# Optimization experiments

Measured on AMD Instinct MI355X. Metric: run time of the kernel, lower is better.

The kernel has to match this reference:

```python
import jax, jax.numpy as jnp
import numpy as np

FC = 2048      # fc_feat_size
VEMB = 512     # video_embedding_size
WEMB = 512     # word_embedding_size
H = 512        # lstm_hidden_size
A = 256        # att_hidden_size
TV = 32        # video_time_step
TC = 20        # caption_time_step
BC = 16        # batch_size_caption
RP = 32        # rp_num (proposals per caption)
B = BC * RP    # batch_size
GLOVE = 300


def setup_inputs() -> dict:
    key = jax.random.key(0)
    ks = jax.random.split(key, 12)
    def u(k, shape):
        return jax.random.uniform(k, shape, jnp.float32, -0.1, 0.1)
    def n(k, shape, s=0.05):
        return jax.random.normal(k, shape, jnp.float32) * s
    return {
        "video_fc_feat": jax.random.normal(ks[0], (B, TV, FC), jnp.float32),
        "video_caption": jax.random.normal(ks[1], (BC, TC, GLOVE), jnp.float32),
        "cap_length_list": jax.random.randint(ks[2], (BC,), 0, TC),
        # video_embedding / word_embedding (Linear layers)
        "W_vemb": u(ks[3], (VEMB, FC)), "b_vemb": jnp.zeros((VEMB,), jnp.float32),
        "W_wemb": u(ks[4], (WEMB, GLOVE)), "b_wemb": jnp.zeros((WEMB,), jnp.float32),
        # LSTMCell for video (gate order i,f,g,o as in torch)
        "Wih_v": n(ks[5], (4 * H, VEMB)), "Whh_v": n(ks[6], (4 * H, H)),
        "bih_v": jnp.zeros((4 * H,), jnp.float32), "bhh_v": jnp.zeros((4 * H,), jnp.float32),
        # LSTMCell for caption
        "Wih_c": n(ks[7], (4 * H, WEMB)), "Whh_c": n(ks[8], (4 * H, H)),
        "bih_c": jnp.zeros((4 * H,), jnp.float32), "bhh_c": jnp.zeros((4 * H,), jnp.float32),
        # attention linears
        "W_vid": u(ks[9], (A, H)), "b_vid": jnp.zeros((A,), jnp.float32),
        "W_sen": u(ks[10], (A, H)), "b_sen": jnp.zeros((A,), jnp.float32),
        "W_att": u(ks[11], (1, A)), "b_att": jnp.zeros((1,), jnp.float32),
    }


def _lstm(x_seq, Wih, Whh, bih, bhh):
    # x_seq: [B, T, D] -> hidden states [B, T, H]; torch LSTMCell gate order i,f,g,o
    Bb = x_seq.shape[0]
    Hh = Whh.shape[1]
    def step(carry, x):
        h, c = carry
        g = x @ Wih.T + bih + h @ Whh.T + bhh
        i, f, gg, o = jnp.split(g, 4, axis=-1)
        c = jax.nn.sigmoid(f) * c + jax.nn.sigmoid(i) * jnp.tanh(gg)
        h = jax.nn.sigmoid(o) * jnp.tanh(c)
        return (h, c), h
    init = (jnp.zeros((Bb, Hh), x_seq.dtype), jnp.zeros((Bb, Hh), x_seq.dtype))
    _, hs = jax.lax.scan(step, init, jnp.swapaxes(x_seq, 0, 1))
    return jnp.swapaxes(hs, 0, 1)


def reference(video_fc_feat, video_caption, cap_length_list,
              W_vemb, b_vemb, W_wemb, b_wemb,
              Wih_v, Whh_v, bih_v, bhh_v,
              Wih_c, Whh_c, bih_c, bhh_c,
              W_vid, b_vid, W_sen, b_sen, W_att, b_att):
    Bb, TVv, _ = video_fc_feat.shape
    BCc, TCc, _ = video_caption.shape
    rp = Bb // BCc
    Hh = Whh_v.shape[1]

    # caption LSTM over embedded GloVe words
    cap_x = video_caption @ W_wemb.T + b_wemb                 # [BC, TC, WEMB]
    cap_h = _lstm(cap_x, Wih_c, Whh_c, bih_c, bhh_c)          # [BC, TC, H]
    # video LSTM over embedded fc features
    vid_x = video_fc_feat @ W_vemb.T + b_vemb                 # [B, TV, VEMB]
    vid_h = _lstm(vid_x, Wih_v, Whh_v, bih_v, bhh_v)          # [B, TV, H]

    # additive attention: tanh(vid_linear(h_v) + sen_linear(h_c)) -> att_linear
    c_lin = cap_h @ W_sen.T + b_sen                           # [BC, TC, A]
    v_lin = (vid_h @ W_vid.T + b_vid).reshape(BCc, rp, TVv, -1)  # [BC, RP, TV, A]
    scores = (jnp.tanh(v_lin[:, :, :, None, :] + c_lin[:, None, None, :, :])
              @ W_att.T + b_att)[..., 0]                      # [BC, RP, TV, TC]

    # ragged masked softmax over caption length (max(len, 1) as in original)
    cap_len = jnp.maximum(cap_length_list, 1)
    mask = jnp.arange(TCc)[None, :] < cap_len[:, None]        # [BC, TC]
    m = mask[:, None, None, :]
    w = jax.nn.softmax(jnp.where(m, scores, -1e9), axis=-1)
    w = jnp.where(m, w, 0.0)                                  # [BC, RP, TV, TC]

    att_cap = jnp.einsum('brvt,bth->brvh', w, cap_h)          # [BC, RP, TV, H]
    cap_ftr_mean = att_cap.mean(axis=2)                       # mean over video steps
    vid_mean = vid_h.mean(axis=1).reshape(BCc, rp, Hh)
    return (vid_mean, cap_ftr_mean)
```

## Files before the change

### kernel.cpp

```cpp
#include <hip/hip_runtime.h>
#include <hip/hip_bf16.h>

#define FCD 2048
#define VEMBD 512
#define WEMBD 512
#define HD 512
#define AD 256
#define TVD 32
#define TCD 20
#define BCD 16
#define RPD 32
#define BD 512
#define GLOVED 300

typedef __attribute__((ext_vector_type(8))) short short8v;
typedef __attribute__((ext_vector_type(4))) float f32x4;

__device__ __forceinline__ float sigf(float x) { return 1.0f / (1.0f + __expf(-x)); }
__device__ __forceinline__ float tanhfast(float x) {
    float e = __expf(2.0f * x);
    return 1.0f - 2.0f / (e + 1.0f);
}
__device__ __forceinline__ unsigned short f2bf(float x) {
    union { __hip_bfloat16 h; unsigned short u; } v;
    v.h = __float2bfloat16(x);
    return v.u;
}
__device__ __forceinline__ float b2f(unsigned short u) {
    union { unsigned int i; float f; } v;
    v.i = ((unsigned int)u) << 16;
    return v.f;
}

__launch_bounds__(256)
__global__ void conv_f2b_kernel(const float* __restrict__ src,
                                unsigned short* __restrict__ dst, int n4) {
    for (int i = blockIdx.x * 256 + threadIdx.x; i < n4; i += gridDim.x * 256) {
        const float4 v = ((const float4*)src)[i];
        ushort4 o;
        o.x = f2bf(v.x); o.y = f2bf(v.y); o.z = f2bf(v.z); o.w = f2bf(v.w);
        ((ushort4*)dst)[i] = o;
    }
}

__launch_bounds__(256)
__global__ void conv_wcat_perm_kernel(const float* __restrict__ Wih,
                                      const float* __restrict__ Whh,
                                      unsigned short* __restrict__ Wcat) {
    const int gp = blockIdx.x;
    const int q = (gp >> 4) & 3;
    const int hc = (gp >> 6) * 16 + (gp & 15);
    const long g = (long)(q * 512 + hc);
    for (int k = threadIdx.x; k < 512; k += 256) {
        Wcat[(long)gp * 1024 + k]       = f2bf(Wih[g * 512 + k]);
        Wcat[(long)gp * 1024 + 512 + k] = f2bf(Whh[g * 512 + k]);
    }
}

__launch_bounds__(256)
__global__ void conv_bsum_kernel(const float* __restrict__ bih,
                                 const float* __restrict__ bhh,
                                 float* __restrict__ bsum) {
    const int gp = blockIdx.x * 256 + threadIdx.x;
    if (gp < 2048) {
        const int q = (gp >> 4) & 3;
        const int hc = (gp >> 6) * 16 + (gp & 15);
        const int g = q * 512 + hc;
        bsum[gp] = bih[g] + bhh[g];
    }
}

template<int AF32, int OBF>
__launch_bounds__(256)
__global__ void mfma_gemm128(const void* __restrict__ A,
                             const unsigned short* __restrict__ Bw,
                             const float* __restrict__ bias,
                             void* __restrict__ Cout,
                             int M, int N, int K)
{
    __shared__ unsigned short As[128][72];
    __shared__ unsigned short Bs[128][72];
    const int m0 = blockIdx.x * 128;
    const int n0 = blockIdx.y * 128;
    const int tid = threadIdx.x;
    const int lane = tid & 63;
    const int wid = tid >> 6;
    const int wm = (wid >> 1) * 64;
    const int wn = (wid & 1) * 64;
    const int lrow = lane & 15;
    const int lko = (lane >> 4) * 8;
    const int sr = tid >> 1;
    const int sc = (tid & 1) * 32;

    f32x4 acc[4][4] = {};

    const float* Arow_f = (const float*)A + (long)(m0 + sr) * K;
    const unsigned short* Arow_b = (const unsigned short*)A + (long)(m0 + sr) * K;
    const unsigned short* Brow = Bw + (long)(n0 + sr) * K;

    if (AF32) {
#pragma unroll
        for (int i = 0; i < 8; i++) {
            const float4 v = *(const float4*)(Arow_f + sc + i * 4);
            unsigned short* d = &As[sr][sc + i * 4];
            d[0] = f2bf(v.x); d[1] = f2bf(v.y); d[2] = f2bf(v.z); d[3] = f2bf(v.w);
        }
    } else {
#pragma unroll
        for (int i = 0; i < 4; i++)
            *(short8v*)&As[sr][sc + i * 8] = *(const short8v*)(Arow_b + sc + i * 8);
    }
#pragma unroll
    for (int i = 0; i < 4; i++)
        *(short8v*)&Bs[sr][sc + i * 8] = *(const short8v*)(Brow + sc + i * 8);
    __syncthreads();

    const int nc = K >> 6;
    float4 paf[8];
    short8v pab[4], pb[4];
    for (int c = 0; c < nc; c++) {
        if (c < nc - 1) {
            const int k0 = (c + 1) * 64;
            if (AF32) {
#pragma unroll
                for (int i = 0; i < 8; i++)
                    paf[i] = *(const float4*)(Arow_f + k0 + sc + i * 4);
            } else {
#pragma unroll
                for (int i = 0; i < 4; i++)
                    pab[i] = *(const short8v*)(Arow_b + k0 + sc + i * 8);
            }
#pragma unroll
            for (int i = 0; i < 4; i++)
                pb[i] = *(const short8v*)(Brow + k0 + sc + i * 8);
        }
#pragma unroll
        for (int kk = 0; kk < 2; kk++) {
            short8v a[4], b[4];
#pragma unroll
            for (int mi = 0; mi < 4; mi++)
                a[mi] = *(const short8v*)&As[wm + mi * 16 + lrow][kk * 32 + lko];
#pragma unroll
            for (int ni = 0; ni < 4; ni++)
                b[ni] = *(const short8v*)&Bs[wn + ni * 16 + lrow][kk * 32 + lko];
#pragma unroll
            for (int mi = 0; mi < 4; mi++)
#pragma unroll
                for (int ni = 0; ni < 4; ni++)
                    acc[mi][ni] = __builtin_amdgcn_mfma_f32_16x16x32_bf16(
                        a[mi], b[ni], acc[mi][ni], 0, 0, 0);
        }
        __syncthreads();
        if (c < nc - 1) {
            if (AF32) {
#pragma unroll
                for (int i = 0; i < 8; i++) {
                    unsigned short* d = &As[sr][sc + i * 4];
                    d[0] = f2bf(paf[i].x); d[1] = f2bf(paf[i].y);
                    d[2] = f2bf(paf[i].z); d[3] = f2bf(paf[i].w);
                }
            } else {
#pragma unroll
                for (int i = 0; i < 4; i++)
                    *(short8v*)&As[sr][sc + i * 8] = pab[i];
            }
#pragma unroll
            for (int i = 0; i < 4; i++)
                *(short8v*)&Bs[sr][sc + i * 8] = pb[i];
            __syncthreads();
        }
    }

    const int rbase = (lane >> 4) * 4;
#pragma unroll
    for (int ni = 0; ni < 4; ni++) {
        const int col = n0 + wn + ni * 16 + lrow;
        const float bv = bias[col];
#pragma unroll
        for (int mi = 0; mi < 4; mi++) {
#pragma unroll
            for (int j = 0; j < 4; j++) {
                const long row = m0 + wm + mi * 16 + rbase + j;
                const float val = acc[mi][ni][j] + bv;
                if (OBF) ((unsigned short*)Cout)[row * N + col] = f2bf(val);
                else     ((float*)Cout)[row * N + col] = val;
            }
        }
    }
}

__launch_bounds__(512)
__global__ void step_fused(const unsigned short* __restrict__ vx,
                           const unsigned short* __restrict__ h_in,
                           unsigned short* __restrict__ h_out,
                           const unsigned short* __restrict__ Wcat,
                           const float* __restrict__ bsum,
                           float* __restrict__ c_state,
                           unsigned short* __restrict__ vid_h,
                           int t,
                           const float* __restrict__ xg,
                           const float* __restrict__ Whh_c,
                           const float* __restrict__ bhh_c,
                           const float* __restrict__ hc_in,
                           float* __restrict__ hc_out,
                           float* __restrict__ cap_cst,
                           float* __restrict__ cap_h)
{
    __shared__ __align__(16) unsigned char smem[69632];
    const int bx = blockIdx.x;
    const int tid = threadIdx.x;

    if (bx >= 256) {
        const int h0 = (bx - 256) * 16;
        float* Wsc = (float*)smem;
        float* Hshc = (float*)(smem + 17408);
        const int lrow = tid >> 3;
        const int lq8 = tid & 7;
        const int tx = tid & 15;
        const int ty = (tid >> 4) & 15;
        float acc4[4] = {};

        for (int k0 = 0; k0 < 512; k0 += 64) {
            {
                const int q = lrow >> 4;
                const int hcc = lrow & 15;
                const float* src = Whh_c + (long)(q * 512 + h0 + hcc) * 512 + k0 + lq8 * 8;
                const int col = hcc * 4 + q;
#pragma unroll
                for (int j = 0; j < 2; j++) {
                    const float4 v = *(const float4*)(src + j * 4);
                    Wsc[(lq8 * 8 + j * 4 + 0) * 68 + col] = v.x;
                    Wsc[(lq8 * 8 + j * 4 + 1) * 68 + col] = v.y;
                    Wsc[(lq8 * 8 + j * 4 + 2) * 68 + col] = v.z;
                    Wsc[(lq8 * 8 + j * 4 + 3) * 68 + col] = v.w;
                }
            }
            if (tid < 256) {
                const int lb = tid >> 4;
                const int lk4 = (tid & 15) * 4;
                *(float4*)&Hshc[lb * 68 + lk4] = *(const float4*)(hc_in + (long)lb * 512 + k0 + lk4);
            }
            __syncthreads();
            if (tid < 256) {
#pragma unroll
                for (int kq = 0; kq < 16; kq++) {
                    const float4 h4 = *(const float4*)&Hshc[ty * 68 + kq * 4];
                    const float4 w0 = *(const float4*)&Wsc[(kq * 4 + 0) * 68 + tx * 4];
                    const float4 w1 = *(const float4*)&Wsc[(kq * 4 + 1) * 68 + tx * 4];
                    const float4 w2 = *(const float4*)&Wsc[(kq * 4 + 2) * 68 + tx * 4];
                    const float4 w3 = *(const float4*)&Wsc[(kq * 4 + 3) * 68 + tx * 4];
                    acc4[0] += h4.x * w0.x + h4.y * w1.x + h4.z * w2.x + h4.w * w3.x;
                    acc4[1] += h4.x * w0.y + h4.y * w1.y + h4.z * w2.y + h4.w * w3.y;
                    acc4[2] += h4.x * w0.z + h4.y * w1.z + h4.z * w2.z + h4.w * w3.z;
                    acc4[3] += h4.x * w0.w + h4.y * w1.w + h4.z * w2.w + h4.w * w3.w;
                }
            }
            __syncthreads();
        }
        if (tid < 256) {
            const int hc = h0 + tx;
            const long xrow = (long)(ty * TCD + t) * 2048;
            const float gi = acc4[0] + xg[xrow + hc]        + bhh_c[hc];
            const float gf = acc4[1] + xg[xrow + 512 + hc]  + bhh_c[512 + hc];
            const float gg = acc4[2] + xg[xrow + 1024 + hc] + bhh_c[1024 + hc];
            const float go = acc4[3] + xg[xrow + 1536 + hc] + bhh_c[1536 + hc];
            const float c_old = cap_cst[(long)ty * 512 + hc];
            const float ii = sigf(gi), ff = sigf(gf), g2 = tanhfast(gg), oo = sigf(go);
            const float c = ff * c_old + ii * g2;
            const float h = oo * tanhfast(c);
            cap_cst[(long)ty * 512 + hc] = c;
            hc_out[(long)ty * 512 + hc] = h;
            cap_h[(long)(ty * TCD + t) * 512 + hc] = h;
        }
        return;
    }

    const int n0 = (bx & 31) * 64;
    const int b0 = (bx >> 5) * 64;
    const int lane = tid & 63;
    const int wl = (tid >> 6) & 3;
    const int g = tid >> 8;
    const int lrow = lane & 15;
    const int lko = (lane >> 4) * 8;
    const int sr = tid >> 3;
    const int sc = (tid & 7) * 16;

    unsigned short* As0 = (unsigned short*)smem;
    unsigned short* Ws0 = (unsigned short*)(smem + 17408);
    unsigned short* As1 = (unsigned short*)(smem + 34816);
    unsigned short* Ws1 = (unsigned short*)(smem + 52224);
    unsigned short* Asg = (unsigned short*)(smem + g * 34816);
    unsigned short* Wsg = Asg + 17408 / 2;

    const unsigned short* arow_vx = vx + ((long)(b0 + sr) * TVD + t) * 512;
    const unsigned short* arow_h  = h_in + (long)(b0 + sr) * 512;
    const unsigned short* wrow    = Wcat + (long)(n0 + sr) * 1024;

    f32x4 acc[4] = {};

#pragma unroll
    for (int i = 0; i < 2; i++) {
        *(short8v*)&As0[sr * 136 + sc + i * 8] = *(const short8v*)(arow_vx + sc + i * 8);
        *(short8v*)&Ws0[sr * 136 + sc + i * 8] = *(const short8v*)(wrow + sc + i * 8);
        *(short8v*)&As1[sr * 136 + sc + i * 8] = *(const short8v*)(arow_h + sc + i * 8);
        *(short8v*)&Ws1[sr * 136 + sc + i * 8] = *(const short8v*)(wrow + 512 + sc + i * 8);
    }
    __syncthreads();

    short8v pa0[2], pw0[2], pa1[2], pw1[2];
    for (int p = 0; p < 4; p++) {
        if (p < 3) {
            const int k0 = (p + 1) * 128;
#pragma unroll
            for (int i = 0; i < 2; i++) {
                pa0[i] = *(const short8v*)(arow_vx + k0 + sc + i * 8);
                pw0[i] = *(const short8v*)(wrow + k0 + sc + i * 8);
                pa1[i] = *(const short8v*)(arow_h + k0 + sc + i * 8);
                pw1[i] = *(const short8v*)(wrow + 512 + k0 + sc + i * 8);
            }
        }
#pragma unroll
        for (int kk = 0; kk < 4; kk++) {
            const short8v a = *(const short8v*)&Asg[(wl * 16 + lrow) * 136 + kk * 32 + lko];
#pragma unroll
            for (int ni = 0; ni < 4; ni++) {
                const short8v b = *(const short8v*)&Wsg[(ni * 16 + lrow) * 136 + kk * 32 + lko];
                acc[ni] = __builtin_amdgcn_mfma_f32_16x16x32_bf16(a, b, acc[ni], 0, 0, 0);
            }
        }
        __syncthreads();
        if (p < 3) {
#pragma unroll
            for (int i = 0; i < 2; i++) {
                *(short8v*)&As0[sr * 136 + sc + i * 8] = pa0[i];
                *(short8v*)&Ws0[sr * 136 + sc + i * 8] = pw0[i];
                *(short8v*)&As1[sr * 136 + sc + i * 8] = pa1[i];
                *(short8v*)&Ws1[sr * 136 + sc + i * 8] = pw1[i];
            }
            __syncthreads();
        }
    }

    float* red = (float*)(smem + 34816);
    const int flat = wl * 64 + lane;
    if (g == 1) {
#pragma unroll
        for (int ni = 0; ni < 4; ni++)
#pragma unroll
            for (int j = 0; j < 4; j++)
                red[(ni * 4 + j) * 256 + flat] = acc[ni][j];
    }
    __syncthreads();
    if (g == 0) {
        const int hc = (n0 >> 2) + lrow;
        const int rbase = (lane >> 4) * 4;
        const float bs0 = bsum[n0 + lrow];
        const float bs1 = bsum[n0 + 16 + lrow];
        const float bs2 = bsum[n0 + 32 + lrow];
        const float bs3 = bsum[n0 + 48 + lrow];
#pragma unroll
        for (int j = 0; j < 4; j++) {
            const long b = b0 + wl * 16 + rbase + j;
            const float gi = acc[0][j] + red[(0 * 4 + j) * 256 + flat] + bs0;
            const float gf = acc[1][j] + red[(1 * 4 + j) * 256 + flat] + bs1;
            const float gg = acc[2][j] + red[(2 * 4 + j) * 256 + flat] + bs2;
            const float go = acc[3][j] + red[(3 * 4 + j) * 256 + flat] + bs3;
            const float c_old = c_state[b * 512 + hc];
            const float ii = sigf(gi), ff = sigf(gf), g2 = tanhfast(gg), oo = sigf(go);
            const float cn = ff * c_old + ii * g2;
            const float h = oo * tanhfast(cn);
            c_state[b * 512 + hc] = cn;
            h_out[b * 512 + hc] = f2bf(h);
            vid_h[(b * TVD + t) * 512 + hc] = f2bf(h);
        }
    }
}

__launch_bounds__(256)
__global__ void gemm_bias_kernel(const float* __restrict__ A,
                                 const float* __restrict__ Bw,
                                 const float* __restrict__ bias,
                                 float* __restrict__ C,
                                 int M, int N, int K) {
    __shared__ float As[16][68];
    __shared__ float Bs[16][68];
    const int n0 = blockIdx.x * 64;
    const int m0 = blockIdx.y * 64;
    const int tid = threadIdx.x;
    const int tx = tid & 15;
    const int ty = tid >> 4;
    const int lrow = tid >> 2;
    const int lk4 = (tid & 3) * 4;

    float acc[4][4] = {};

    for (int k0 = 0; k0 < K; k0 += 16) {
        {
            const float* src = A + (long)(m0 + lrow) * K + k0 + lk4;
            float4 v;
            if (k0 + 16 <= K) v = *(const float4*)src;
            else {
                v.x = (k0 + lk4 + 0 < K) ? src[0] : 0.f;
                v.y = (k0 + lk4 + 1 < K) ? src[1] : 0.f;
                v.z = (k0 + lk4 + 2 < K) ? src[2] : 0.f;
                v.w = (k0 + lk4 + 3 < K) ? src[3] : 0.f;
            }
            As[lk4 + 0][lrow] = v.x; As[lk4 + 1][lrow] = v.y;
            As[lk4 + 2][lrow] = v.z; As[lk4 + 3][lrow] = v.w;
        }
        {
            const float* src = Bw + (long)(n0 + lrow) * K + k0 + lk4;
            float4 v;
            if (k0 + 16 <= K) v = *(const float4*)src;
            else {
                v.x = (k0 + lk4 + 0 < K) ? src[0] : 0.f;
                v.y = (k0 + lk4 + 1 < K) ? src[1] : 0.f;
                v.z = (k0 + lk4 + 2 < K) ? src[2] : 0.f;
                v.w = (k0 + lk4 + 3 < K) ? src[3] : 0.f;
            }
            Bs[lk4 + 0][lrow] = v.x; Bs[lk4 + 1][lrow] = v.y;
            Bs[lk4 + 2][lrow] = v.z; Bs[lk4 + 3][lrow] = v.w;
        }
        __syncthreads();
#pragma unroll
        for (int kk = 0; kk < 16; kk++) {
            const float4 av = *(const float4*)&As[kk][ty * 4];
            const float4 bv = *(const float4*)&Bs[kk][tx * 4];
            acc[0][0] += av.x * bv.x; acc[0][1] += av.x * bv.y; acc[0][2] += av.x * bv.z; acc[0][3] += av.x * bv.w;
            acc[1][0] += av.y * bv.x; acc[1][1] += av.y * bv.y; acc[1][2] += av.y * bv.z; acc[1][3] += av.y * bv.w;
            acc[2][0] += av.z * bv.x; acc[2][1] += av.z * bv.y; acc[2][2] += av.z * bv.z; acc[2][3] += av.z * bv.w;
            acc[3][0] += av.w * bv.x; acc[3][1] += av.w * bv.y; acc[3][2] += av.w * bv.z; acc[3][3] += av.w * bv.w;
        }
        __syncthreads();
    }

    const float b0v = bias[n0 + tx * 4 + 0];
    const float b1v = bias[n0 + tx * 4 + 1];
    const float b2v = bias[n0 + tx * 4 + 2];
    const float b3v = bias[n0 + tx * 4 + 3];
#pragma unroll
    for (int i = 0; i < 4; i++) {
        float* dst = C + (long)(m0 + ty * 4 + i) * N + n0 + tx * 4;
        dst[0] = acc[i][0] + b0v;
        dst[1] = acc[i][1] + b1v;
        dst[2] = acc[i][2] + b2v;
        dst[3] = acc[i][3] + b3v;
    }
}

__launch_bounds__(256)
__global__ void attn_kernel(const float* __restrict__ v_lin,
                            const float* __restrict__ c_lin,
                            const float* __restrict__ W_att,
                            const float* __restrict__ b_att,
                            const int* __restrict__ cap_len,
                            float* __restrict__ wbar)
{
    const int br = blockIdx.x;
    const int bc = br >> 5;
    const int tid = threadIdx.x;
    const int lane = tid & 63;
    const int wv = tid >> 6;
    __shared__ float cl[TCD][AD];
    __shared__ float vl[AD];
    __shared__ float sl[TVD][TCD];

    for (int tt = 0; tt < TCD; tt++)
        cl[tt][tid] = c_lin[(long)(bc * TCD + tt) * AD + tid];
    const float wa0 = W_att[lane];
    const float wa1 = W_att[64 + lane];
    const float wa2 = W_att[128 + lane];
    const float wa3 = W_att[192 + lane];
    const float batt = b_att[0];
    __syncthreads();

    for (int v = 0; v < TVD; v++) {
        vl[tid] = v_lin[((long)br * TVD + v) * AD + tid];
        __syncthreads();
        const float v0 = vl[lane], v1 = vl[64 + lane], v2 = vl[128 + lane], v3 = vl[192 + lane];
#pragma unroll
        for (int dt = 0; dt < 5; dt++) {
            const int t = wv * 5 + dt;
            float s = tanhfast(v0 + cl[t][lane]) * wa0
                    + tanhfast(v1 + cl[t][64 + lane]) * wa1
                    + tanhfast(v2 + cl[t][128 + lane]) * wa2
                    + tanhfast(v3 + cl[t][192 + lane]) * wa3;
            for (int off = 32; off > 0; off >>= 1) s += __shfl_down(s, off, 64);
            if (lane == 0) sl[v][t] = s + batt;
        }
        __syncthreads();
    }

    int L = cap_len[bc];
    if (L < 1) L = 1;
    if (tid < TVD) {
        const int v = tid;
        float m = -1e30f;
        for (int t = 0; t < TCD; t++)
            if (t < L) m = fmaxf(m, sl[v][t]);
        float sum = 0.f;
        for (int t = 0; t < TCD; t++)
            if (t < L) sum += __expf(sl[v][t] - m);
        const float inv = 1.f / sum;
        for (int t = 0; t < TCD; t++)
            sl[v][t] = (t < L) ? __expf(sl[v][t] - m) * inv : 0.f;
    }
    __syncthreads();
    if (tid < TCD) {
        float s = 0.f;
        for (int v = 0; v < TVD; v++) s += sl[v][tid];
        wbar[(long)br * TCD + tid] = s * (1.0f / TVD);
    }
}

__launch_bounds__(256)
__global__ void capftr_kernel(const float* __restrict__ wbar,
                              const float* __restrict__ cap_h,
                              float* __restrict__ out2)
{
    const int idx = blockIdx.x * 256 + threadIdx.x;
    const int h = idx & 511;
    const int br = idx >> 9;
    const int bc = br >> 5;
    float s = 0.f;
#pragma unroll
    for (int t = 0; t < TCD; t++)
        s += wbar[br * TCD + t] * cap_h[(long)(bc * TCD + t) * HD + h];
    out2[idx] = s;
}

__launch_bounds__(256)
__global__ void vidmean_bf_kernel(const unsigned short* __restrict__ vid_h,
                                  float* __restrict__ out1)
{
    const int idx = blockIdx.x * 256 + threadIdx.x;
    const int b = idx >> 6;
    const int h8 = (idx & 63) * 8;
    float s[8] = {};
    for (int t = 0; t < TVD; t++) {
        const short8v v = *(const short8v*)(vid_h + ((long)b * TVD + t) * 512 + h8);
#pragma unroll
        for (int j = 0; j < 8; j++) s[j] += b2f((unsigned short)v[j]);
    }
#pragma unroll
    for (int j = 0; j < 8; j++)
        out1[(long)b * 512 + h8 + j] = s[j] * (1.0f / TVD);
}

extern "C" void kernel_launch(void* const* d_in, const int* in_sizes, int n_in,
                              void* d_out, int out_size, void* d_ws, size_t ws_size,
                              hipStream_t stream) {
    const float* video_fc      = (const float*)d_in[0];
    const float* video_caption = (const float*)d_in[1];
    const int*   cap_len       = (const int*)d_in[2];
    const float* W_vemb = (const float*)d_in[3];
    const float* b_vemb = (const float*)d_in[4];
    const float* W_wemb = (const float*)d_in[5];
    const float* b_wemb = (const float*)d_in[6];
    const float* Wih_v  = (const float*)d_in[7];
    const float* Whh_v  = (const float*)d_in[8];
    const float* bih_v  = (const float*)d_in[9];
    const float* bhh_v  = (const float*)d_in[10];
    const float* Wih_c  = (const float*)d_in[11];
    const float* Whh_c  = (const float*)d_in[12];
    const float* bih_c  = (const float*)d_in[13];
    const float* bhh_c  = (const float*)d_in[14];
    const float* W_vid  = (const float*)d_in[15];
    const float* b_vid  = (const float*)d_in[16];
    const float* W_sen  = (const float*)d_in[17];
    const float* b_sen  = (const float*)d_in[18];
    const float* W_att  = (const float*)d_in[19];
    const float* b_att  = (const float*)d_in[20];

    float* out1 = (float*)d_out;
    float* out2 = out1 + BD * HD;

    float* ws = (float*)d_ws;
    size_t off = 0;
    auto alloc = [&](size_t nfloats) {
        float* p = ws + off;
        off += (nfloats + 63) & ~(size_t)63;
        return p;
    };
    unsigned short* vidx_bf = (unsigned short*)alloc((size_t)BD * TVD * VEMBD / 2);
    unsigned short* vidh_bf = (unsigned short*)alloc((size_t)BD * TVD * HD / 2);
    unsigned short* h_bf_a  = (unsigned short*)alloc((size_t)BD * HD / 2);
    unsigned short* h_bf_b  = (unsigned short*)alloc((size_t)BD * HD / 2);
    float* c_st    = alloc((size_t)BD * HD);
    float* v_lin   = alloc((size_t)BD * TVD * AD);
    unsigned short* Wvemb_bf = (unsigned short*)alloc((size_t)VEMBD * FCD / 2);
    unsigned short* Wvid_bf  = (unsigned short*)alloc((size_t)AD * HD / 2);
    unsigned short* Wcat_bf  = (unsigned short*)alloc((size_t)2048 * 1024 / 2);
    float* bsum    = alloc(2048);
    float* cap_x   = alloc((size_t)BCD * TCD * WEMBD);
    float* xg_c    = alloc((size_t)BCD * TCD * 4 * HD);
    float* cap_h   = alloc((size_t)BCD * TCD * HD);
    float* c_lin   = alloc((size_t)BCD * TCD * AD);
    float* wbar    = alloc((size_t)BD * TCD);
    float* cap_ha  = alloc((size_t)BCD * HD);
    float* cap_hb  = alloc((size_t)BCD * HD);
    float* cap_cst = alloc((size_t)BCD * HD);

    hipMemsetAsync(h_bf_a, 0, (size_t)BD * HD * sizeof(unsigned short), stream);
    hipMemsetAsync(c_st, 0, (size_t)BD * HD * sizeof(float), stream);
    hipMemsetAsync(cap_ha, 0, (size_t)BCD * HD * sizeof(float), stream);
    hipMemsetAsync(cap_cst, 0, (size_t)BCD * HD * sizeof(float), stream);

    conv_f2b_kernel<<<512, 256, 0, stream>>>(W_vemb, Wvemb_bf, VEMBD * FCD / 4);
    conv_f2b_kernel<<<128, 256, 0, stream>>>(W_vid, Wvid_bf, AD * HD / 4);
    conv_wcat_perm_kernel<<<2048, 256, 0, stream>>>(Wih_v, Whh_v, Wcat_bf);
    conv_bsum_kernel<<<8, 256, 0, stream>>>(bih_v, bhh_v, bsum);

    gemm_bias_kernel<<<dim3(WEMBD / 64, (BCD * TCD) / 64), 256, 0, stream>>>(
        video_caption, W_wemb, b_wemb, cap_x, BCD * TCD, WEMBD, GLOVED);
    gemm_bias_kernel<<<dim3((4 * HD) / 64, (BCD * TCD) / 64), 256, 0, stream>>>(
        cap_x, Wih_c, bih_c, xg_c, BCD * TCD, 4 * HD, WEMBD);

    mfma_gemm128<1, 1><<<dim3((BD * TVD) / 128, VEMBD / 128), 256, 0, stream>>>(
        video_fc, Wvemb_bf, b_vemb, vidx_bf, BD * TVD, VEMBD, FCD);

    for (int t = 0; t < TVD; t++) {
        const unsigned short* hin = (t & 1) ? h_bf_b : h_bf_a;
        unsigned short* hout = (t & 1) ? h_bf_a : h_bf_b;
        const float* chin = (t & 1) ? cap_hb : cap_ha;
        float* chout = (t & 1) ? cap_ha : cap_hb;
        const int nblk = (t < TCD) ? 288 : 256;
        step_fused<<<nblk, 512, 0, stream>>>(
            vidx_bf, hin, hout, Wcat_bf, bsum, c_st, vidh_bf, t,
            xg_c, Whh_c, bhh_c, chin, chout, cap_cst, cap_h);
    }

    gemm_bias_kernel<<<dim3(AD / 64, (BCD * TCD) / 64), 256, 0, stream>>>(
        cap_h, W_sen, b_sen, c_lin, BCD * TCD, AD, HD);
    mfma_gemm128<0, 0><<<dim3((BD * TVD) / 128, AD / 128), 256, 0, stream>>>(
        vidh_bf, Wvid_bf, b_vid, v_lin, BD * TVD, AD, HD);

    attn_kernel<<<BD, 256, 0, stream>>>(v_lin, c_lin, W_att, b_att, cap_len, wbar);
    capftr_kernel<<<(BD * HD) / 256, 256, 0, stream>>>(wbar, cap_h, out2);
    vidmean_bf_kernel<<<(BD * HD / 8) / 256, 256, 0, stream>>>(vidh_bf, out1);
}
```

Before: 884.2 us.

## Shrink LSTM step blocks to 256 threads, fuse capftr into attention, preconvert fc feats

The recurrent step kernel moves from 512-thread blocks with a split-K reduction over 64-row tiles to 256-thread blocks on 32-row batch tiles. Each wave now owns distinct output columns, and the smem footprint drops so two blocks fit per CU. The caption-feature weighted sum is folded into the attention kernel, removing one launch and the wbar buffer. When workspace allows, video_fc is converted to bf16 first so the embedding GEMM reads bf16 input, at the cost of an extra conversion pass over a large tensor.

New measurement: 847.5 us. -4.1%, faster.

```diff
diff --git a/kernel.cpp b/kernel.cpp
--- a/kernel.cpp
+++ b/kernel.cpp
@@ -189,7 +189,7 @@
     }
 }
 
-__launch_bounds__(512)
+__launch_bounds__(256, 2)
 __global__ void step_fused(const unsigned short* __restrict__ vx,
                            const unsigned short* __restrict__ h_in,
                            unsigned short* __restrict__ h_out,
@@ -206,165 +206,157 @@
                            float* __restrict__ cap_cst,
                            float* __restrict__ cap_h)
 {
-    __shared__ __align__(16) unsigned char smem[69632];
+    __shared__ __align__(16) unsigned char smem[26112];
     const int bx = blockIdx.x;
     const int tid = threadIdx.x;
 
-    if (bx >= 256) {
-        const int h0 = (bx - 256) * 16;
+    if (bx >= 512) {
+        const int h0 = (bx - 512) * 16;
         float* Wsc = (float*)smem;
         float* Hshc = (float*)(smem + 17408);
-        const int lrow = tid >> 3;
-        const int lq8 = tid & 7;
         const int tx = tid & 15;
-        const int ty = (tid >> 4) & 15;
+        const int ty = tid >> 4;
+        const int lrow2 = tid >> 2;
+        const int lq = tid & 3;
         float acc4[4] = {};
 
         for (int k0 = 0; k0 < 512; k0 += 64) {
             {
-                const int q = lrow >> 4;
-                const int hcc = lrow & 15;
-                const float* src = Whh_c + (long)(q * 512 + h0 + hcc) * 512 + k0 + lq8 * 8;
+                const int q = lrow2 >> 4;
+                const int hcc = lrow2 & 15;
+                const float* src = Whh_c + (long)(q * 512 + h0 + hcc) * 512 + k0 + lq * 16;
                 const int col = hcc * 4 + q;
 #pragma unroll
-                for (int j = 0; j < 2; j++) {
+                for (int j = 0; j < 4; j++) {
                     const float4 v = *(const float4*)(src + j * 4);
-                    Wsc[(lq8 * 8 + j * 4 + 0) * 68 + col] = v.x;
-                    Wsc[(lq8 * 8 + j * 4 + 1) * 68 + col] = v.y;
-                    Wsc[(lq8 * 8 + j * 4 + 2) * 68 + col] = v.z;
-                    Wsc[(lq8 * 8 + j * 4 + 3) * 68 + col] = v.w;
+                    Wsc[(lq * 16 + j * 4 + 0) * 68 + col] = v.x;
+                    Wsc[(lq * 16 + j * 4 + 1) * 68 + col] = v.y;
+                    Wsc[(lq * 16 + j * 4 + 2) * 68 + col] = v.z;
+                    Wsc[(lq * 16 + j * 4 + 3) * 68 + col] = v.w;
                 }
             }
-            if (tid < 256) {
+            {
                 const int lb = tid >> 4;
                 const int lk4 = (tid & 15) * 4;
                 *(float4*)&Hshc[lb * 68 + lk4] = *(const float4*)(hc_in + (long)lb * 512 + k0 + lk4);
             }
             __syncthreads();
-            if (tid < 256) {
-#pragma unroll
-                for (int kq = 0; kq < 16; kq++) {
-                    const float4 h4 = *(const float4*)&Hshc[ty * 68 + kq * 4];
-                    const float4 w0 = *(const float4*)&Wsc[(kq * 4 + 0) * 68 + tx * 4];
-                    const float4 w1 = *(const float4*)&Wsc[(kq * 4 + 1) * 68 + tx * 4];
-                    const float4 w2 = *(const float4*)&Wsc[(kq * 4 + 2) * 68 + tx * 4];
-                    const float4 w3 = *(const float4*)&Wsc[(kq * 4 + 3) * 68 + tx * 4];
-                    acc4[0] += h4.x * w0.x + h4.y * w1.x + h4.z * w2.x + h4.w * w3.x;
-                    acc4[1] += h4.x * w0.y + h4.y * w1.y + h4.z * w2.y + h4.w * w3.y;
-                    acc4[2] += h4.x * w0.z + h4.y * w1.z + h4.z * w2.z + h4.w * w3.z;
-                    acc4[3] += h4.x * w0.w + h4.y * w1.w + h4.z * w2.w + h4.w * w3.w;
-                }
+#pragma unroll
+            for (int kq = 0; kq < 16; kq++) {
+                const float4 h4 = *(const float4*)&Hshc[ty * 68 + kq * 4];
+                const float4 w0 = *(const float4*)&Wsc[(kq * 4 + 0) * 68 + tx * 4];
+                const float4 w1 = *(const float4*)&Wsc[(kq * 4 + 1) * 68 + tx * 4];
+                const float4 w2 = *(const float4*)&Wsc[(kq * 4 + 2) * 68 + tx * 4];
+                const float4 w3 = *(const float4*)&Wsc[(kq * 4 + 3) * 68 + tx * 4];
+                acc4[0] += h4.x * w0.x + h4.y * w1.x + h4.z * w2.x + h4.w * w3.x;
+                acc4[1] += h4.x * w0.y + h4.y * w1.y + h4.z * w2.y + h4.w * w3.y;
+                acc4[2] += h4.x * w0.z + h4.y * w1.z + h4.z * w2.z + h4.w * w3.z;
+                acc4[3] += h4.x * w0.w + h4.y * w1.w + h4.z * w2.w + h4.w * w3.w;
             }
             __syncthreads();
         }
-        if (tid < 256) {
-            const int hc = h0 + tx;
-            const long xrow = (long)(ty * TCD + t) * 2048;
-            const float gi = acc4[0] + xg[xrow + hc]        + bhh_c[hc];
-            const float gf = acc4[1] + xg[xrow + 512 + hc]  + bhh_c[512 + hc];
-            const float gg = acc4[2] + xg[xrow + 1024 + hc] + bhh_c[1024 + hc];
-            const float go = acc4[3] + xg[xrow + 1536 + hc] + bhh_c[1536 + hc];
-            const float c_old = cap_cst[(long)ty * 512 + hc];
-            const float ii = sigf(gi), ff = sigf(gf), g2 = tanhfast(gg), oo = sigf(go);
-            const float c = ff * c_old + ii * g2;
-            const float h = oo * tanhfast(c);
-            cap_cst[(long)ty * 512 + hc] = c;
-            hc_out[(long)ty * 512 + hc] = h;
-            cap_h[(long)(ty * TCD + t) * 512 + hc] = h;
-        }
+        const int hc = h0 + tx;
+        const long xrow = (long)(ty * TCD + t) * 2048;
+        const float gi = acc4[0] + xg[xrow + hc]        + bhh_c[hc];
+        const float gf = acc4[1] + xg[xrow + 512 + hc]  + bhh_c[512 + hc];
+        const float gg = acc4[2] + xg[xrow + 1024 + hc] + bhh_c[1024 + hc];
+        const float go = acc4[3] + xg[xrow + 1536 + hc] + bhh_c[1536 + hc];
+        const float c_old = cap_cst[(long)ty * 512 + hc];
+        const float ii = sigf(gi), ff = sigf(gf), g2 = tanhfast(gg), oo = sigf(go);
+        const float c = ff * c_old + ii * g2;
+        const float h = oo * tanhfast(c);
+        cap_cst[(long)ty * 512 + hc] = c;
+        hc_out[(long)ty * 512 + hc] = h;
+        cap_h[(long)(ty * TCD + t) * 512 + hc] = h;
         return;
     }
 
     const int n0 = (bx & 31) * 64;
-    const int b0 = (bx >> 5) * 64;
+    const int b0 = (bx >> 5) * 32;
     const int lane = tid & 63;
-    const int wl = (tid >> 6) & 3;
-    const int g = tid >> 8;
+    const int w = tid >> 6;
+    const int bi = w & 1;
+    const int nq = w >> 1;
     const int lrow = lane & 15;
     const int lko = (lane >> 4) * 8;
-    const int sr = tid >> 3;
-    const int sc = (tid & 7) * 16;
-
-    unsigned short* As0 = (unsigned short*)smem;
-    unsigned short* Ws0 = (unsigned short*)(smem + 17408);
-    unsigned short* As1 = (unsigned short*)(smem + 34816);
-    unsigned short* Ws1 = (unsigned short*)(smem + 52224);
-    unsigned short* Asg = (unsigned short*)(smem + g * 34816);
-    unsigned short* Wsg = Asg + 17408 / 2;
-
-    const unsigned short* arow_vx = vx + ((long)(b0 + sr) * TVD + t) * 512;
-    const unsigned short* arow_h  = h_in + (long)(b0 + sr) * 512;
-    const unsigned short* wrow    = Wcat + (long)(n0 + sr) * 1024;
-
-    f32x4 acc[4] = {};
-
-#pragma unroll
-    for (int i = 0; i < 2; i++) {
-        *(short8v*)&As0[sr * 136 + sc + i * 8] = *(const short8v*)(arow_vx + sc + i * 8);
-        *(short8v*)&Ws0[sr * 136 + sc + i * 8] = *(const short8v*)(wrow + sc + i * 8);
-        *(short8v*)&As1[sr * 136 + sc + i * 8] = *(const short8v*)(arow_h + sc + i * 8);
-        *(short8v*)&Ws1[sr * 136 + sc + i * 8] = *(const short8v*)(wrow + 512 + sc + i * 8);
-    }
+    const int sra = tid >> 3;
+    const int sca = (tid & 7) * 16;
+
+    unsigned short* As = (unsigned short*)smem;
+    unsigned short* Ws = (unsigned short*)(smem + 8704);
+
+    const unsigned short* arow_vx = vx + ((long)(b0 + sra) * TVD + t) * 512;
+    const unsigned short* arow_h  = h_in + (long)(b0 + sra) * 512;
+    const unsigned short* wrow0   = Wcat + (long)(n0 + sra) * 1024;
+    const unsigned short* wrow1   = Wcat + (long)(n0 + sra + 32) * 1024;
+
+    f32x4 acc[2] = {};
+
+    *(short8v*)&As[sra * 136 + sca]     = *(const short8v*)(arow_vx + sca);
+    *(short8v*)&As[sra * 136 + sca + 8] = *(const short8v*)(arow_vx + sca + 8);
+    *(short8v*)&Ws[sra * 136 + sca]            = *(const short8v*)(wrow0 + sca);
+    *(short8v*)&Ws[sra * 136 + sca + 8]        = *(const short8v*)(wrow0 + sca + 8);
+    *(short8v*)&Ws[(sra + 32) * 136 + sca]     = *(const short8v*)(wrow1 + sca);
+    *(short8v*)&Ws[(sra + 32) * 136 + sca + 8] = *(const short8v*)(wrow1 + sca + 8);
     __syncthreads();
 
-    short8v pa0[2], pw0[2], pa1[2], pw1[2];
-    for (int p = 0; p < 4; p++) {
-        if (p < 3) {
-            const int k0 = (p + 1) * 128;
-#pragma unroll
-            for (int i = 0; i < 2; i++) {
-                pa0[i] = *(const short8v*)(arow_vx + k0 + sc + i * 8);
-                pw0[i] = *(const short8v*)(wrow + k0 + sc + i * 8);
-                pa1[i] = *(const short8v*)(arow_h + k0 + sc + i * 8);
-                pw1[i] = *(const short8v*)(wrow + 512 + k0 + sc + i * 8);
-            }
+    short8v pa0, pa1, pw0, pw1, pw2, pw3;
+    for (int c = 0; c < 8; c++) {
+        if (c < 7) {
+            const int k0 = (c + 1) * 128;
+            const unsigned short* ap = (k0 < 512) ? (arow_vx + k0) : (arow_h + (k0 - 512));
+            pa0 = *(const short8v*)(ap + sca);
+            pa1 = *(const short8v*)(ap + sca + 8);
+            pw0 = *(const short8v*)(wrow0 + k0 + sca);
+            pw1 = *(const short8v*)(wrow0 + k0 + sca + 8);
+            pw2 = *(const short8v*)(wrow1 + k0 + sca);
+            pw3 = *(const short8v*)(wrow1 + k0 + sca + 8);
         }
 #pragma unroll
         for (int kk = 0; kk < 4; kk++) {
-            const short8v a = *(const short8v*)&Asg[(wl * 16 + lrow) * 136 + kk * 32 + lko];
-#pragma unroll
-            for (int ni = 0; ni < 4; ni++) {
-                const short8v b = *(const short8v*)&Wsg[(ni * 16 + lrow) * 136 + kk * 32 + lko];
-                acc[ni] = __builtin_amdgcn_mfma_f32_16x16x32_bf16(a, b, acc[ni], 0, 0, 0);
+            const short8v a = *(const short8v*)&As[(bi * 16 + lrow) * 136 + kk * 32 + lko];
+#pragma unroll
+            for (int nl = 0; nl < 2; nl++) {
+                const short8v b = *(const short8v*)&Ws[((nq * 2 + nl) * 16 + lrow) * 136 + kk * 32 + lko];
+                acc[nl] = __builtin_amdgcn_mfma_f32_16x16x32_bf16(a, b, acc[nl], 0, 0, 0);
             }
         }
         __syncthreads();
-        if (p < 3) {
-#pragma unroll
-            for (int i = 0; i < 2; i++) {
-                *(short8v*)&As0[sr * 136 + sc + i * 8] = pa0[i];
-                *(short8v*)&Ws0[sr * 136 + sc + i * 8] = pw0[i];
-                *(short8v*)&As1[sr * 136 + sc + i * 8] = pa1[i];
-                *(short8v*)&Ws1[sr * 136 + sc + i * 8] = pw1[i];
-            }
+        if (c < 7) {
+            *(short8v*)&As[sra * 136 + sca]            = pa0;
+            *(short8v*)&As[sra * 136 + sca + 8]        = pa1;
+            *(short8v*)&Ws[sra * 136 + sca]            = pw0;
+            *(short8v*)&Ws[sra * 136 + sca + 8]        = pw1;
+            *(short8v*)&Ws[(sra + 32) * 136 + sca]     = pw2;
+            *(short8v*)&Ws[(sra + 32) * 136 + sca + 8] = pw3;
             __syncthreads();
         }
     }
 
-    float* red = (float*)(smem + 34816);
-    const int flat = wl * 64 + lane;
-    if (g == 1) {
-#pragma unroll
-        for (int ni = 0; ni < 4; ni++)
+    float* red = (float*)smem;
+    const int rbase = (lane >> 4) * 4;
+    if (w >= 2) {
+#pragma unroll
+        for (int nl = 0; nl < 2; nl++)
 #pragma unroll
             for (int j = 0; j < 4; j++)
-                red[(ni * 4 + j) * 256 + flat] = acc[ni][j];
+                red[nl * 512 + (bi * 16 + rbase + j) * 16 + lrow] = acc[nl][j];
     }
     __syncthreads();
-    if (g == 0) {
+    if (w < 2) {
         const int hc = (n0 >> 2) + lrow;
-        const int rbase = (lane >> 4) * 4;
         const float bs0 = bsum[n0 + lrow];
         const float bs1 = bsum[n0 + 16 + lrow];
         const float bs2 = bsum[n0 + 32 + lrow];
         const float bs3 = bsum[n0 + 48 + lrow];
 #pragma unroll
         for (int j = 0; j < 4; j++) {
-            const long b = b0 + wl * 16 + rbase + j;
-            const float gi = acc[0][j] + red[(0 * 4 + j) * 256 + flat] + bs0;
-            const float gf = acc[1][j] + red[(1 * 4 + j) * 256 + flat] + bs1;
-            const float gg = acc[2][j] + red[(2 * 4 + j) * 256 + flat] + bs2;
-            const float go = acc[3][j] + red[(3 * 4 + j) * 256 + flat] + bs3;
+            const int blocal = bi * 16 + rbase + j;
+            const long b = b0 + blocal;
+            const float gi = acc[0][j] + bs0;
+            const float gf = acc[1][j] + bs1;
+            const float gg = red[blocal * 16 + lrow] + bs2;
+            const float go = red[512 + blocal * 16 + lrow] + bs3;
             const float c_old = c_state[b * 512 + hc];
             const float ii = sigf(gi), ff = sigf(gf), g2 = tanhfast(gg), oo = sigf(go);
             const float cn = ff * c_old + ii * g2;
@@ -454,7 +446,8 @@
                             const float* __restrict__ W_att,
                             const float* __restrict__ b_att,
                             const int* __restrict__ cap_len,
-                            float* __restrict__ wbar)
+                            const float* __restrict__ cap_h,
+                            float* __restrict__ out2)
 {
     const int br = blockIdx.x;
     const int bc = br >> 5;
@@ -464,6 +457,7 @@
     __shared__ float cl[TCD][AD];
     __shared__ float vl[AD];
     __shared__ float sl[TVD][TCD];
+    __shared__ float wsum[TCD];
 
     for (int tt = 0; tt < TCD; tt++)
         cl[tt][tid] = c_lin[(long)(bc * TCD + tt) * AD + tid];
@@ -509,24 +503,20 @@
     if (tid < TCD) {
         float s = 0.f;
         for (int v = 0; v < TVD; v++) s += sl[v][tid];
-        wbar[(long)br * TCD + tid] = s * (1.0f / TVD);
-    }
-}
-
-__launch_bounds__(256)
-__global__ void capftr_kernel(const float* __restrict__ wbar,
-                              const float* __restrict__ cap_h,
-                              float* __restrict__ out2)
-{
-    const int idx = blockIdx.x * 256 + threadIdx.x;
-    const int h = idx & 511;
-    const int br = idx >> 9;
-    const int bc = br >> 5;
-    float s = 0.f;
-#pragma unroll
-    for (int t = 0; t < TCD; t++)
-        s += wbar[br * TCD + t] * cap_h[(long)(bc * TCD + t) * HD + h];
-    out2[idx] = s;
+        wsum[tid] = s * (1.0f / TVD);
+    }
+    __syncthreads();
+
+    const float* chb = cap_h + (long)bc * TCD * HD;
+#pragma unroll
+    for (int r = 0; r < 2; r++) {
+        const int h = r * 256 + tid;
+        float s = 0.f;
+#pragma unroll
+        for (int t = 0; t < TCD; t++)
+            s += wsum[t] * chb[t * HD + h];
+        out2[(long)br * HD + h] = s;
+    }
 }
 
 __launch_bounds__(256)
@@ -596,10 +586,12 @@
     float* xg_c    = alloc((size_t)BCD * TCD * 4 * HD);
     float* cap_h   = alloc((size_t)BCD * TCD * HD);
     float* c_lin   = alloc((size_t)BCD * TCD * AD);
-    float* wbar    = alloc((size_t)BD * TCD);
     float* cap_ha  = alloc((size_t)BCD * HD);
     float* cap_hb  = alloc((size_t)BCD * HD);
     float* cap_cst = alloc((size_t)BCD * HD);
+    const size_t fcn = (size_t)BD * TVD * FCD;
+    const bool preconv = ((off + fcn / 2 + 64) * sizeof(float) <= ws_size);
+    unsigned short* vidfc_bf = preconv ? (unsigned short*)alloc(fcn / 2) : nullptr;
 
     hipMemsetAsync(h_bf_a, 0, (size_t)BD * HD * sizeof(unsigned short), stream);
     hipMemsetAsync(c_st, 0, (size_t)BD * HD * sizeof(float), stream);
@@ -616,16 +608,22 @@
     gemm_bias_kernel<<<dim3((4 * HD) / 64, (BCD * TCD) / 64), 256, 0, stream>>>(
         cap_x, Wih_c, bih_c, xg_c, BCD * TCD, 4 * HD, WEMBD);
 
-    mfma_gemm128<1, 1><<<dim3((BD * TVD) / 128, VEMBD / 128), 256, 0, stream>>>(
-        video_fc, Wvemb_bf, b_vemb, vidx_bf, BD * TVD, VEMBD, FCD);
+    if (preconv) {
+        conv_f2b_kernel<<<2048, 256, 0, stream>>>(video_fc, vidfc_bf, (int)(fcn / 4));
+        mfma_gemm128<0, 1><<<dim3((BD * TVD) / 128, VEMBD / 128), 256, 0, stream>>>(
+            vidfc_bf, Wvemb_bf, b_vemb, vidx_bf, BD * TVD, VEMBD, FCD);
+    } else {
+        mfma_gemm128<1, 1><<<dim3((BD * TVD) / 128, VEMBD / 128), 256, 0, stream>>>(
+            video_fc, Wvemb_bf, b_vemb, vidx_bf, BD * TVD, VEMBD, FCD);
+    }
 
     for (int t = 0; t < TVD; t++) {
         const unsigned short* hin = (t & 1) ? h_bf_b : h_bf_a;
         unsigned short* hout = (t & 1) ? h_bf_a : h_bf_b;
         const float* chin = (t & 1) ? cap_hb : cap_ha;
         float* chout = (t & 1) ? cap_ha : cap_hb;
-        const int nblk = (t < TCD) ? 288 : 256;
-        step_fused<<<nblk, 512, 0, stream>>>(
+        const int nblk = (t < TCD) ? 544 : 512;
+        step_fused<<<nblk, 256, 0, stream>>>(
             vidx_bf, hin, hout, Wcat_bf, bsum, c_st, vidh_bf, t,
             xg_c, Whh_c, bhh_c, chin, chout, cap_cst, cap_h);
     }
@@ -635,7 +633,6 @@
     mfma_gemm128<0, 0><<<dim3((BD * TVD) / 128, AD / 128), 256, 0, stream>>>(
         vidh_bf, Wvid_bf, b_vid, v_lin, BD * TVD, AD, HD);
 
-    attn_kernel<<<BD, 256, 0, stream>>>(v_lin, c_lin, W_att, b_att, cap_len, wbar);
-    capftr_kernel<<<(BD * HD) / 256, 256, 0, stream>>>(wbar, cap_h, out2);
+    attn_kernel<<<BD, 256, 0, stream>>>(v_lin, c_lin, W_att, b_att, cap_len, cap_h, out2);
     vidmean_bf_kernel<<<(BD * HD / 8) / 256, 256, 0, stream>>>(vidh_bf, out1);
 }
```
